# Performance work log

Measured on AMD Instinct MI355X. Metric: run time of the kernel, lower is better.

Reference implementation:

```python
import jax, jax.numpy as jnp
import numpy as np

ENCODER_DIM = 512
HIDDEN_DIM = 512
ATTENTION_DIM = 512
BATCH = 512
NUM_PIXELS = 196


def setup_inputs() -> dict:
    key = jax.random.key(0)
    ks = jax.random.split(key, 8)
    s_enc = 1.0 / np.sqrt(ENCODER_DIM)
    s_dec = 1.0 / np.sqrt(HIDDEN_DIM)
    s_att = 1.0 / np.sqrt(ATTENTION_DIM)
    return {
        "encoder_out": jax.random.normal(ks[0], (BATCH, NUM_PIXELS, ENCODER_DIM), jnp.float32),
        "decoder_hidden": jax.random.normal(ks[1], (BATCH, HIDDEN_DIM), jnp.float32),
        # enc_att: Linear(encoder_dim -> attention_dim)
        "W_enc": jax.random.uniform(ks[2], (ENCODER_DIM, ATTENTION_DIM), jnp.float32, -s_enc, s_enc),
        "b_enc": jax.random.uniform(ks[3], (ATTENTION_DIM,), jnp.float32, -s_enc, s_enc),
        # dec_att: Linear(hidden_dim -> attention_dim)
        "W_dec": jax.random.uniform(ks[4], (HIDDEN_DIM, ATTENTION_DIM), jnp.float32, -s_dec, s_dec),
        "b_dec": jax.random.uniform(ks[5], (ATTENTION_DIM,), jnp.float32, -s_dec, s_dec),
        # full_att: Linear(attention_dim -> 1)
        "w_full": jax.random.uniform(ks[6], (ATTENTION_DIM,), jnp.float32, -s_att, s_att),
        "b_full": jax.random.uniform(ks[7], (1,), jnp.float32, -s_att, s_att),
    }


def reference(encoder_out, decoder_hidden, W_enc, b_enc, W_dec, b_dec, w_full, b_full):
    # att_enc: [B, P, A]
    att_enc = jnp.einsum('bpe,ea->bpa', encoder_out, W_enc) + b_enc
    # att_dec: [B, 1, A]
    att_dec = (decoder_hidden @ W_dec + b_dec)[:, None, :]
    # energy: [B, P]
    energy = jnp.einsum('bpa,a->bp', jax.nn.relu(att_enc + att_dec), w_full) + b_full[0]
    alpha = jax.nn.softmax(energy, axis=1)  # [B, P]
    context = jnp.einsum('bpe,bp->be', encoder_out, alpha)  # [B, E]
    return context, alpha
```

## Files before the change

### kernel.cpp

```cpp
#include <hip/hip_runtime.h>
#include <hip/hip_bf16.h>
#include <cstdint>

#define KDIM 512
#define BM 256
#define BN 256
#define BK 64
#define M_MAIN 100352
#define NPIX 196
#define BATCH 512

typedef float f32x4 __attribute__((ext_vector_type(4)));
typedef short s16x8 __attribute__((ext_vector_type(8)));

__device__ __forceinline__ short f2bf(float f) {
    uint32_t u = __float_as_uint(f);
    uint32_t r = u + 0x7FFFu + ((u >> 16) & 1u);
    return (short)(r >> 16);
}

__device__ __forceinline__ void gload_lds16(const void* g, void* l) {
    __builtin_amdgcn_global_load_lds(
        (const __attribute__((address_space(1))) void*)g,
        (__attribute__((address_space(3))) void*)l, 16, 0, 0);
}

__device__ __forceinline__ uint32_t pkbf(float lo, float hi) {
    __hip_bfloat162 p = __float22bfloat162_rn(float2{lo, hi});
    return *reinterpret_cast<uint32_t*>(&p);
}

__global__ void prep_w(const float* __restrict__ W_enc, const float* __restrict__ W_dec,
                       short* __restrict__ Wt_enc, short* __restrict__ Wt_dec) {
    int a = blockIdx.x;
    int k = threadIdx.x;
    const float* W = blockIdx.y ? W_dec : W_enc;
    short* Wt = blockIdx.y ? Wt_dec : Wt_enc;
    Wt[a * KDIM + k] = f2bf(W[(size_t)k * KDIM + a]);
}

template <int EPI>
__launch_bounds__(512, 2)
__global__ void gemm_fused(const float* __restrict__ A, int M,
                           const short* __restrict__ Bt,
                           const float* __restrict__ b1, const float* __restrict__ b2,
                           const float* __restrict__ attdec, const float* __restrict__ wfull,
                           float* __restrict__ outp) {
    __shared__ short lds_a[2][BM][BK];
    __shared__ short lds_b[2][BN][BK];

    const int tid = threadIdx.x;
    const int wave = tid >> 6;
    const int lane = tid & 63;
    const int wm = wave >> 2;
    const int wn = wave & 3;
    const int nwg = gridDim.x;
    int swzb;
    if ((nwg & 7) == 0) {
        int q = nwg >> 3;
        swzb = (blockIdx.x & 7) * q + (blockIdx.x >> 3);
    } else {
        swzb = blockIdx.x;
    }
    const int bx = swzb & 1;
    const int by = swzb >> 1;
    const int r0 = by * BM;
    const int c0 = bx * BN;

    f32x4 areg[4][2];

    auto loadA = [&](int kt) {
#pragma unroll
        for (int j = 0; j < 4; ++j) {
            int g = tid + 512 * j;
            int row = g >> 3, col8 = (g & 7) * 8;
            const float* p = A + (size_t)(r0 + row) * KDIM + kt * BK + col8;
            areg[j][0] = *(const f32x4*)p;
            areg[j][1] = *(const f32x4*)(p + 4);
        }
    };
    auto writeA = [&](int buf) {
#pragma unroll
        for (int j = 0; j < 4; ++j) {
            int g = tid + 512 * j;
            int row = g >> 3;
            int slot = (g & 7) ^ (row & 7);
            uint4 w;
            w.x = pkbf(areg[j][0][0], areg[j][0][1]);
            w.y = pkbf(areg[j][0][2], areg[j][0][3]);
            w.z = pkbf(areg[j][1][0], areg[j][1][1]);
            w.w = pkbf(areg[j][1][2], areg[j][1][3]);
            *reinterpret_cast<uint4*>(&lds_a[buf][row][slot * 8]) = w;
        }
    };
    auto stageB = [&](int buf, int kt) {
#pragma unroll
        for (int i = 0; i < 4; ++i) {
            int rb = wave * 32 + i * 8;
            int srcslot = (lane & 7) ^ (lane >> 3);
            const short* g = Bt + (size_t)(c0 + rb + (lane >> 3)) * KDIM + kt * BK + srcslot * 8;
            gload_lds16(g, &lds_b[buf][rb][0]);
        }
    };

    f32x4 acc[8][4];
#pragma unroll
    for (int i = 0; i < 8; ++i)
#pragma unroll
        for (int j = 0; j < 4; ++j)
            acc[i][j] = (f32x4){0.f, 0.f, 0.f, 0.f};

    s16x8 af[8], bf[4];
    auto readFrags = [&](int buf, int kk) {
#pragma unroll
        for (int fm = 0; fm < 8; ++fm) {
            int ra = wm * 128 + fm * 16 + (lane & 15);
            int sl = (kk * 4 + (lane >> 4)) ^ (ra & 7);
            af[fm] = *(const s16x8*)&lds_a[buf][ra][sl * 8];
        }
#pragma unroll
        for (int fn = 0; fn < 4; ++fn) {
            int rb = wn * 64 + fn * 16 + (lane & 15);
            int sl = (kk * 4 + (lane >> 4)) ^ (rb & 7);
            bf[fn] = *(const s16x8*)&lds_b[buf][rb][sl * 8];
        }
    };
    auto mfmaAll = [&]() {
        __builtin_amdgcn_s_setprio(1);
#pragma unroll
        for (int fm = 0; fm < 8; ++fm)
#pragma unroll
            for (int fn = 0; fn < 4; ++fn)
                acc[fm][fn] = __builtin_amdgcn_mfma_f32_16x16x32_bf16(af[fm], bf[fn], acc[fm][fn], 0, 0, 0);
        __builtin_amdgcn_s_setprio(0);
    };

    loadA(0);
    __builtin_amdgcn_sched_barrier(0);
    stageB(0, 0);
    __builtin_amdgcn_sched_barrier(0);
    writeA(0);
    loadA(1);
    __builtin_amdgcn_sched_barrier(0);
    asm volatile("s_waitcnt vmcnt(8)" ::: "memory");
    asm volatile("s_waitcnt lgkmcnt(0)" ::: "memory");
    __builtin_amdgcn_s_barrier();

    const int nk = KDIM / BK;
    for (int t = 0; t < nk - 1; ++t) {
        const int cur = t & 1;
        stageB(cur ^ 1, t + 1);
        __builtin_amdgcn_sched_barrier(0);
        readFrags(cur, 0);
        writeA(cur ^ 1);
        mfmaAll();
        readFrags(cur, 1);
        loadA(t + 2 < nk ? t + 2 : nk - 1);
        __builtin_amdgcn_sched_barrier(0);
        mfmaAll();
        asm volatile("s_waitcnt vmcnt(8)" ::: "memory");
        asm volatile("s_waitcnt lgkmcnt(0)" ::: "memory");
        __builtin_amdgcn_s_barrier();
    }
    readFrags(1, 0);
    mfmaAll();
    readFrags(1, 1);
    mfmaAll();

    const int lcol = lane & 15;
    const int lrg = (lane >> 4) * 4;

    if constexpr (EPI == 0) {
#pragma unroll
        for (int fm = 0; fm < 8; ++fm)
#pragma unroll
            for (int fn = 0; fn < 4; ++fn) {
                int col = c0 + wn * 64 + fn * 16 + lcol;
                float bias = b1[col] + b2[col];
#pragma unroll
                for (int reg = 0; reg < 4; ++reg) {
                    int row = r0 + wm * 128 + fm * 16 + lrg + reg;
                    outp[(size_t)row * KDIM + col] = acc[fm][fn][reg] + bias;
                }
            }
    } else {
        float wfv[4];
        int colv[4];
#pragma unroll
        for (int fn = 0; fn < 4; ++fn) {
            colv[fn] = c0 + wn * 64 + fn * 16 + lcol;
            wfv[fn] = wfull[colv[fn]];
        }
        float* ebuf = reinterpret_cast<float*>(lds_a);
#pragma unroll
        for (int fm = 0; fm < 8; ++fm) {
#pragma unroll
            for (int reg = 0; reg < 4; ++reg) {
                int rl = wm * 128 + fm * 16 + lrg + reg;
                int row = r0 + rl;
                int b = row / NPIX;
                float es = 0.f;
#pragma unroll
                for (int fn = 0; fn < 4; ++fn) {
                    float v = acc[fm][fn][reg] + attdec[(size_t)b * KDIM + colv[fn]];
                    v = fmaxf(v, 0.f);
                    es = fmaf(v, wfv[fn], es);
                }
#pragma unroll
                for (int m = 1; m < 16; m <<= 1) es += __shfl_xor(es, m);
                if (lcol == 0) ebuf[wn * BM + rl] = es;
            }
        }
        __syncthreads();
        if (tid < BM) {
            float s = (ebuf[tid] + ebuf[BM + tid]) + (ebuf[2 * BM + tid] + ebuf[3 * BM + tid]);
            outp[(size_t)bx * M + r0 + tid] = s;
        }
    }
}

__global__ void softmax_ctx(const float* __restrict__ enc, const float* __restrict__ energy2,
                            float* __restrict__ out) {
    const int b = blockIdx.x;
    const int t = threadIdx.x;
    __shared__ float sal[NPIX];
    __shared__ float wred[4];

    float e = -1e30f;
    if (t < NPIX)
        e = energy2[b * NPIX + t] + energy2[(size_t)M_MAIN + b * NPIX + t];
    float m = e;
#pragma unroll
    for (int d = 1; d < 64; d <<= 1) m = fmaxf(m, __shfl_xor(m, d));
    if ((t & 63) == 0) wred[t >> 6] = m;
    __syncthreads();
    m = fmaxf(fmaxf(wred[0], wred[1]), fmaxf(wred[2], wred[3]));

    float ex = (t < NPIX) ? __expf(e - m) : 0.f;
    float sm = ex;
#pragma unroll
    for (int d = 1; d < 64; d <<= 1) sm += __shfl_xor(sm, d);
    __syncthreads();
    if ((t & 63) == 0) wred[t >> 6] = sm;
    __syncthreads();
    sm = wred[0] + wred[1] + wred[2] + wred[3];

    float al = ex / sm;
    if (t < NPIX) {
        sal[t] = al;
        out[BATCH * KDIM + b * NPIX + t] = al;
    }
    __syncthreads();

    float c0 = 0.f, c1 = 0.f;
    const float* eb = enc + (size_t)b * NPIX * KDIM;
    const int col = 2 * t;
#pragma unroll 4
    for (int p = 0; p < NPIX; ++p) {
        float a = sal[p];
        float2 v = *(const float2*)(eb + (size_t)p * KDIM + col);
        c0 = fmaf(v.x, a, c0);
        c1 = fmaf(v.y, a, c1);
    }
    out[b * KDIM + col] = c0;
    out[b * KDIM + col + 1] = c1;
}

extern "C" void kernel_launch(void* const* d_in, const int* in_sizes, int n_in,
                              void* d_out, int out_size, void* d_ws, size_t ws_size,
                              hipStream_t stream) {
    const float* encoder = (const float*)d_in[0];
    const float* dec_h   = (const float*)d_in[1];
    const float* W_enc   = (const float*)d_in[2];
    const float* b_enc   = (const float*)d_in[3];
    const float* W_dec   = (const float*)d_in[4];
    const float* b_decv  = (const float*)d_in[5];
    const float* w_full  = (const float*)d_in[6];
    float* out = (float*)d_out;

    short* wt_enc = (short*)d_ws;
    short* wt_dec = wt_enc + 512 * 512;
    float* attdec = (float*)(wt_dec + 512 * 512);
    float* energy2 = attdec + 512 * 512;

    prep_w<<<dim3(512, 2), 512, 0, stream>>>(W_enc, W_dec, wt_enc, wt_dec);

    gemm_fused<0><<<dim3(4), 512, 0, stream>>>(dec_h, 512, wt_dec,
                                               b_enc, b_decv, nullptr, nullptr, attdec);

    gemm_fused<1><<<dim3(2 * (M_MAIN / BM)), 512, 0, stream>>>(encoder, M_MAIN, wt_enc,
                                                               nullptr, nullptr, attdec, w_full, energy2);

    softmax_ctx<<<dim3(BATCH), 256, 0, stream>>>(encoder, energy2, out);
}
```

Baseline: 161.8 us.

## Split GEMM main loop into four ping-pong phases with interleaved loads

Restructures the bf16 MFMA main loop into four sub-phases per K tile. Each phase reads half of the A fragments and issues half of the B/A global staging, then runs 16 MFMAs between workgroup barriers, so memory traffic and compute alternate across waves in a ping-pong style. This halves the A fragment registers, which may help occupancy, but adds several extra s_barrier and lgkmcnt waits per iteration that could serialize waves.

```diff
diff --git a/kernel.cpp b/kernel.cpp
--- a/kernel.cpp
+++ b/kernel.cpp
@@ -12,6 +12,11 @@
 
 typedef float f32x4 __attribute__((ext_vector_type(4)));
 typedef short s16x8 __attribute__((ext_vector_type(8)));
+
+#define SCHED0 __builtin_amdgcn_sched_barrier(0)
+#define BARRIER __builtin_amdgcn_s_barrier()
+#define WAIT_LGKM0 asm volatile("s_waitcnt lgkmcnt(0)" ::: "memory")
+#define WAIT_VM8 asm volatile("s_waitcnt vmcnt(8)" ::: "memory")
 
 __device__ __forceinline__ short f2bf(float f) {
     uint32_t u = __float_as_uint(f);
@@ -69,9 +74,9 @@
 
     f32x4 areg[4][2];
 
-    auto loadA = [&](int kt) {
-#pragma unroll
-        for (int j = 0; j < 4; ++j) {
+    auto loadA_half = [&](int kt, int h) {
+#pragma unroll
+        for (int j = 2 * h; j < 2 * h + 2; ++j) {
             int g = tid + 512 * j;
             int row = g >> 3, col8 = (g & 7) * 8;
             const float* p = A + (size_t)(r0 + row) * KDIM + kt * BK + col8;
@@ -79,9 +84,9 @@
             areg[j][1] = *(const f32x4*)(p + 4);
         }
     };
-    auto writeA = [&](int buf) {
-#pragma unroll
-        for (int j = 0; j < 4; ++j) {
+    auto writeA_half = [&](int buf, int h) {
+#pragma unroll
+        for (int j = 2 * h; j < 2 * h + 2; ++j) {
             int g = tid + 512 * j;
             int row = g >> 3;
             int slot = (g & 7) ^ (row & 7);
@@ -93,9 +98,9 @@
             *reinterpret_cast<uint4*>(&lds_a[buf][row][slot * 8]) = w;
         }
     };
-    auto stageB = [&](int buf, int kt) {
-#pragma unroll
-        for (int i = 0; i < 4; ++i) {
+    auto stageB_half = [&](int buf, int kt, int h) {
+#pragma unroll
+        for (int i = 2 * h; i < 2 * h + 2; ++i) {
             int rb = wave * 32 + i * 8;
             int srcslot = (lane & 7) ^ (lane >> 3);
             const short* g = Bt + (size_t)(c0 + rb + (lane >> 3)) * KDIM + kt * BK + srcslot * 8;
@@ -110,62 +115,88 @@
         for (int j = 0; j < 4; ++j)
             acc[i][j] = (f32x4){0.f, 0.f, 0.f, 0.f};
 
-    s16x8 af[8], bf[4];
-    auto readFrags = [&](int buf, int kk) {
-#pragma unroll
-        for (int fm = 0; fm < 8; ++fm) {
-            int ra = wm * 128 + fm * 16 + (lane & 15);
+    s16x8 af[4], bf[4];
+    auto dsReadA4 = [&](int buf, int kk, int fmh) {
+#pragma unroll
+        for (int i = 0; i < 4; ++i) {
+            int ra = wm * 128 + (fmh * 4 + i) * 16 + (lane & 15);
             int sl = (kk * 4 + (lane >> 4)) ^ (ra & 7);
-            af[fm] = *(const s16x8*)&lds_a[buf][ra][sl * 8];
-        }
-#pragma unroll
-        for (int fn = 0; fn < 4; ++fn) {
-            int rb = wn * 64 + fn * 16 + (lane & 15);
+            af[i] = *(const s16x8*)&lds_a[buf][ra][sl * 8];
+        }
+    };
+    auto dsReadB4 = [&](int buf, int kk) {
+#pragma unroll
+        for (int i = 0; i < 4; ++i) {
+            int rb = wn * 64 + i * 16 + (lane & 15);
             int sl = (kk * 4 + (lane >> 4)) ^ (rb & 7);
-            bf[fn] = *(const s16x8*)&lds_b[buf][rb][sl * 8];
-        }
-    };
-    auto mfmaAll = [&]() {
+            bf[i] = *(const s16x8*)&lds_b[buf][rb][sl * 8];
+        }
+    };
+    auto mfma16 = [&](int fmh) {
         __builtin_amdgcn_s_setprio(1);
 #pragma unroll
-        for (int fm = 0; fm < 8; ++fm)
-#pragma unroll
-            for (int fn = 0; fn < 4; ++fn)
-                acc[fm][fn] = __builtin_amdgcn_mfma_f32_16x16x32_bf16(af[fm], bf[fn], acc[fm][fn], 0, 0, 0);
+        for (int i = 0; i < 4; ++i)
+#pragma unroll
+            for (int j = 0; j < 4; ++j)
+                acc[fmh * 4 + i][j] =
+                    __builtin_amdgcn_mfma_f32_16x16x32_bf16(af[i], bf[j], acc[fmh * 4 + i][j], 0, 0, 0);
         __builtin_amdgcn_s_setprio(0);
     };
 
-    loadA(0);
-    __builtin_amdgcn_sched_barrier(0);
-    stageB(0, 0);
-    __builtin_amdgcn_sched_barrier(0);
-    writeA(0);
-    loadA(1);
-    __builtin_amdgcn_sched_barrier(0);
-    asm volatile("s_waitcnt vmcnt(8)" ::: "memory");
-    asm volatile("s_waitcnt lgkmcnt(0)" ::: "memory");
-    __builtin_amdgcn_s_barrier();
+    loadA_half(0, 0); loadA_half(0, 1);
+    SCHED0;
+    stageB_half(0, 0, 0); stageB_half(0, 0, 1);
+    SCHED0;
+    writeA_half(0, 0); writeA_half(0, 1);
+    loadA_half(1, 0); loadA_half(1, 1);
+    SCHED0;
+    WAIT_VM8;
+    WAIT_LGKM0;
+    SCHED0;
+    BARRIER;
 
     const int nk = KDIM / BK;
     for (int t = 0; t < nk - 1; ++t) {
         const int cur = t & 1;
-        stageB(cur ^ 1, t + 1);
-        __builtin_amdgcn_sched_barrier(0);
-        readFrags(cur, 0);
-        writeA(cur ^ 1);
-        mfmaAll();
-        readFrags(cur, 1);
-        loadA(t + 2 < nk ? t + 2 : nk - 1);
-        __builtin_amdgcn_sched_barrier(0);
-        mfmaAll();
-        asm volatile("s_waitcnt vmcnt(8)" ::: "memory");
-        asm volatile("s_waitcnt lgkmcnt(0)" ::: "memory");
-        __builtin_amdgcn_s_barrier();
-    }
-    readFrags(1, 0);
-    mfmaAll();
-    readFrags(1, 1);
-    mfmaAll();
+        const int nxt = cur ^ 1;
+        const int tA = (t + 2 < nk) ? t + 2 : nk - 1;
+        dsReadB4(cur, 0);
+        dsReadA4(cur, 0, 0);
+        stageB_half(nxt, t + 1, 0);
+        SCHED0; BARRIER; WAIT_LGKM0; SCHED0;
+        mfma16(0);
+        SCHED0; BARRIER;
+        dsReadA4(cur, 0, 1);
+        stageB_half(nxt, t + 1, 1);
+        SCHED0; BARRIER; WAIT_LGKM0; SCHED0;
+        mfma16(1);
+        SCHED0; BARRIER;
+        dsReadB4(cur, 1);
+        dsReadA4(cur, 1, 0);
+        writeA_half(nxt, 0);
+        loadA_half(tA, 0);
+        SCHED0; BARRIER; WAIT_LGKM0; SCHED0;
+        mfma16(0);
+        SCHED0; BARRIER;
+        dsReadA4(cur, 1, 1);
+        writeA_half(nxt, 1);
+        loadA_half(tA, 1);
+        SCHED0; BARRIER; WAIT_LGKM0; SCHED0;
+        mfma16(1);
+        SCHED0;
+        WAIT_LGKM0;
+        WAIT_VM8;
+        SCHED0;
+        BARRIER;
+    }
+    dsReadB4(1, 0); dsReadA4(1, 0, 0);
+    SCHED0; BARRIER; WAIT_LGKM0; SCHED0; mfma16(0); SCHED0; BARRIER;
+    dsReadA4(1, 0, 1);
+    SCHED0; BARRIER; WAIT_LGKM0; SCHED0; mfma16(1); SCHED0; BARRIER;
+    dsReadB4(1, 1); dsReadA4(1, 1, 0);
+    SCHED0; BARRIER; WAIT_LGKM0; SCHED0; mfma16(0); SCHED0; BARRIER;
+    dsReadA4(1, 1, 1);
+    SCHED0; BARRIER; WAIT_LGKM0; SCHED0; mfma16(1);
 
     const int lcol = lane & 15;
     const int lrg = (lane >> 4) * 4;
```

Result: slower. 171.2 us (+5.8%).
